# Optimization experiments

Measured on AMD Instinct MI355X. Metric: run time of the kernel, lower is better.

Reference implementation:

```python
import jax, jax.numpy as jnp
import numpy as np

EPS_SUM = 1e-5   # clamp on soft-assignment mass
EPS_NORM = 1e-12  # F.normalize eps


def setup_inputs() -> dict:
    key = jax.random.key(0)
    k1, k2, k3 = jax.random.split(key, 3)
    bs, ch, h, w = 64, 256, 56, 56
    num_parts = 3
    featmaps = jax.random.normal(k1, (bs, ch, h, w), dtype=jnp.float32)
    # kaiming-normal-like init for centers, clamped positive as in init_parameters
    part_centers = jnp.clip(
        jax.random.normal(k2, (num_parts, ch), dtype=jnp.float32) * np.sqrt(2.0 / ch),
        1e-5, None)
    part_smooth_factors = jax.random.normal(k3, (num_parts,), dtype=jnp.float32) * 0.1
    return {"featmaps": featmaps, "part_centers": part_centers,
            "part_smooth_factors": part_smooth_factors}


def reference(featmaps, part_centers, part_smooth_factors):
    bs, ch, h, w = featmaps.shape
    k = part_centers.shape[0]
    x = featmaps.reshape(bs, ch, h * w)                      # [bs, ch, n]

    # distance terms
    cx = jnp.einsum('kc,bcn->bkn', part_centers, x)          # [bs, k, n]
    x_sq = jnp.sum(x * x, axis=1, keepdims=True)             # [bs, 1, n]
    c_sq = jnp.sum(part_centers * part_centers, axis=1)      # [k]

    beta = jax.nn.sigmoid(part_smooth_factors)               # [k]
    logits = jnp.minimum(2.0 * cx - x_sq - c_sq[None, :, None], 0.0) / beta[None, :, None]
    assign = jax.nn.softmax(logits, axis=1)                  # softmax over parts, [bs, k, n]

    # weighted pooling
    qx = jnp.einsum('bkn,bcn->bkc', assign, x)               # [bs, k, ch]
    sum_ass = jnp.maximum(jnp.sum(assign, axis=2, keepdims=True), EPS_SUM)  # [bs, k, 1]
    qx_ = qx / sum_ass

    sigma = jnp.sqrt(beta / 2.0)                             # [k]
    out = (qx_ - part_centers[None]) / sigma[None, :, None]  # [bs, k, ch]
    norm = jnp.maximum(jnp.linalg.norm(out, axis=2, keepdims=True), EPS_NORM)
    outputs = (out / norm).transpose(0, 2, 1)                # [bs, ch, k]

    return outputs, assign.reshape(bs, k, h, w)
```

## Files before the change

kernel.cpp:

```cpp
#include <hip/hip_runtime.h>
#include <math.h>

#define BS   64
#define CH   256
#define NPIX 3136
#define NK   3

#define WS_CSQ   0
#define WS_RB    4
#define WS_CTR4  8
#define WS_SA    (8 + CH*4)
#define WS_QX    (WS_SA + BS*NK)

__global__ __launch_bounds__(64)
void pgn_setup(const float* __restrict__ centers, const float* __restrict__ psf,
               float* __restrict__ ws)
{
    const int lane = threadIdx.x;
    float4* ctr4 = (float4*)(ws + WS_CTR4);
    #pragma unroll
    for (int j = 0; j < 4; ++j) {
        const int c = lane * 4 + j;
        ctr4[c] = make_float4(centers[c], centers[CH + c], centers[2*CH + c], 0.f);
    }
    #pragma unroll
    for (int k = 0; k < NK; ++k) {
        float s = 0.f;
        #pragma unroll
        for (int j = 0; j < 4; ++j) {
            const float u = centers[k*CH + lane*4 + j];
            s = fmaf(u, u, s);
        }
        #pragma unroll
        for (int m = 32; m; m >>= 1) s += __shfl_xor(s, m, 64);
        if (lane == 0) ws[WS_CSQ + k] = s;
    }
    if (lane < NK) ws[WS_RB + lane] = 1.f + __expf(-psf[lane]);
}

#define TILE1 256
#define NT1   13

__global__ __launch_bounds__(256)
void pgn_assign(const float* __restrict__ x,
                const float* __restrict__ ws,
                float* __restrict__ assign_out,
                float* __restrict__ sa)
{
    __shared__ float4 ctr[CH];
    const int tid = threadIdx.x;
    const int b   = blockIdx.x / NT1;
    const int t   = blockIdx.x % NT1;
    const int n   = t * TILE1 + tid;

    ctr[tid] = ((const float4*)(ws + WS_CTR4))[tid];
    __syncthreads();

    const float cs0 = ws[WS_CSQ+0], cs1 = ws[WS_CSQ+1], cs2 = ws[WS_CSQ+2];
    const float rb0 = ws[WS_RB+0],  rb1 = ws[WS_RB+1],  rb2 = ws[WS_RB+2];

    float a0 = 0.f, a1 = 0.f, a2 = 0.f;
    if (n < NPIX) {
        const float* xb = x + (size_t)b * CH * NPIX + n;
        float c0 = 0.f, c1 = 0.f, c2 = 0.f, xs = 0.f;
        #pragma unroll 8
        for (int c = 0; c < CH; ++c) {
            const float  xv = xb[(size_t)c * NPIX];
            const float4 cc = ctr[c];
            c0 = fmaf(cc.x, xv, c0);
            c1 = fmaf(cc.y, xv, c1);
            c2 = fmaf(cc.z, xv, c2);
            xs = fmaf(xv, xv, xs);
        }
        const float l0 = fminf(2.f*c0 - xs - cs0, 0.f) * rb0;
        const float l1 = fminf(2.f*c1 - xs - cs1, 0.f) * rb1;
        const float l2 = fminf(2.f*c2 - xs - cs2, 0.f) * rb2;
        const float m  = fmaxf(l0, fmaxf(l1, l2));
        const float e0 = __expf(l0 - m), e1 = __expf(l1 - m), e2 = __expf(l2 - m);
        const float inv = 1.f / (e0 + e1 + e2);
        a0 = e0 * inv; a1 = e1 * inv; a2 = e2 * inv;

        float* ao = assign_out + (size_t)b * NK * NPIX + n;
        ao[0]        = a0;
        ao[NPIX]     = a1;
        ao[2*NPIX]   = a2;
    }

    float s0 = a0, s1 = a1, s2 = a2;
    #pragma unroll
    for (int m = 32; m; m >>= 1) {
        s0 += __shfl_xor(s0, m, 64);
        s1 += __shfl_xor(s1, m, 64);
        s2 += __shfl_xor(s2, m, 64);
    }
    if ((tid & 63) == 0) {
        atomicAdd(&sa[b*NK + 0], s0);
        atomicAdd(&sa[b*NK + 1], s1);
        atomicAdd(&sa[b*NK + 2], s2);
    }
}

#define CPB 8
#define NCB (CH/CPB)

__global__ __launch_bounds__(256)
void pgn_pool(const float* __restrict__ x,
              const float* __restrict__ assign,
              float* __restrict__ qx)
{
    const int tid = threadIdx.x;
    const int b   = blockIdx.x / NCB;
    const int c0  = (blockIdx.x % NCB) * CPB;

    const float* ab = assign + (size_t)b * NK * NPIX;
    const float* xb = x + ((size_t)b * CH + c0) * NPIX;

    float q[CPB][NK];
    #pragma unroll
    for (int j = 0; j < CPB; ++j)
        #pragma unroll
        for (int k = 0; k < NK; ++k) q[j][k] = 0.f;

    for (int p = tid * 4; p + 3 < NPIX; p += 256 * 4) {
        const float4 A0 = *(const float4*)(ab + p);
        const float4 A1 = *(const float4*)(ab + NPIX + p);
        const float4 A2 = *(const float4*)(ab + 2*NPIX + p);
        #pragma unroll
        for (int j = 0; j < CPB; ++j) {
            const float4 xv = *(const float4*)(xb + (size_t)j * NPIX + p);
            q[j][0] = fmaf(A0.x, xv.x, fmaf(A0.y, xv.y, fmaf(A0.z, xv.z, fmaf(A0.w, xv.w, q[j][0]))));
            q[j][1] = fmaf(A1.x, xv.x, fmaf(A1.y, xv.y, fmaf(A1.z, xv.z, fmaf(A1.w, xv.w, q[j][1]))));
            q[j][2] = fmaf(A2.x, xv.x, fmaf(A2.y, xv.y, fmaf(A2.z, xv.z, fmaf(A2.w, xv.w, q[j][2]))));
        }
    }

    __shared__ float part[4][CPB*NK];
    const int wave = tid >> 6, lane = tid & 63;
    #pragma unroll
    for (int j = 0; j < CPB; ++j)
        #pragma unroll
        for (int k = 0; k < NK; ++k) {
            float v = q[j][k];
            #pragma unroll
            for (int m = 32; m; m >>= 1) v += __shfl_xor(v, m, 64);
            if (lane == 0) part[wave][j*NK + k] = v;
        }
    __syncthreads();
    if (tid < CPB*NK) {
        const float tot = part[0][tid] + part[1][tid] + part[2][tid] + part[3][tid];
        const int j = tid / NK, k = tid % NK;
        qx[((size_t)b*NK + k)*CH + c0 + j] = tot;
    }
}

__global__ __launch_bounds__(256)
void pgn_final(const float* __restrict__ ws,
               const float* __restrict__ centers,
               const float* __restrict__ psf,
               float* __restrict__ out)
{
    const int b = blockIdx.x;
    const int c = threadIdx.x;
    const int wave = c >> 6, lane = c & 63;
    __shared__ float red[4][NK];
    __shared__ float nrm[NK];

    const float* qx = ws + WS_QX;
    const float* sa = ws + WS_SA;

    float v[NK], ss[NK];
    #pragma unroll
    for (int k = 0; k < NK; ++k) {
        const float beta = 1.f / (1.f + __expf(-psf[k]));
        const float sig  = sqrtf(0.5f * beta);
        const float s    = fmaxf(sa[b*NK + k], 1e-5f);
        const float q    = qx[((size_t)b*NK + k)*CH + c] / s;
        v[k]  = (q - centers[k*CH + c]) / sig;
        ss[k] = v[k] * v[k];
    }
    #pragma unroll
    for (int m = 32; m; m >>= 1) {
        ss[0] += __shfl_xor(ss[0], m, 64);
        ss[1] += __shfl_xor(ss[1], m, 64);
        ss[2] += __shfl_xor(ss[2], m, 64);
    }
    if (lane == 0) { red[wave][0] = ss[0]; red[wave][1] = ss[1]; red[wave][2] = ss[2]; }
    __syncthreads();
    if (c < NK) {
        const float tot = red[0][c] + red[1][c] + red[2][c] + red[3][c];
        nrm[c] = fmaxf(sqrtf(tot), 1e-12f);
    }
    __syncthreads();
    float* o = out + ((size_t)b*CH + c)*NK;
    #pragma unroll
    for (int k = 0; k < NK; ++k) o[k] = v[k] / nrm[k];
}

extern "C" void kernel_launch(void* const* d_in, const int* in_sizes, int n_in,
                              void* d_out, int out_size, void* d_ws, size_t ws_size,
                              hipStream_t stream)
{
    const float* feat    = (const float*)d_in[0];
    const float* centers = (const float*)d_in[1];
    const float* psf     = (const float*)d_in[2];

    float* out        = (float*)d_out;
    float* assign_out = out + (size_t)BS*CH*NK;

    float* ws = (float*)d_ws;
    float* sa = ws + WS_SA;
    float* qx = ws + WS_QX;

    hipMemsetAsync(sa, 0, BS*NK*sizeof(float), stream);

    pgn_setup<<<dim3(1), dim3(64), 0, stream>>>(centers, psf, ws);
    pgn_assign<<<dim3(BS*NT1), dim3(256), 0, stream>>>(feat, ws, assign_out, sa);
    pgn_pool<<<dim3(BS*NCB), dim3(256), 0, stream>>>(feat, assign_out, qx);
    pgn_final<<<dim3(BS), dim3(256), 0, stream>>>(ws, centers, psf, out);
}
```

Before: 335.6 us.

## Fuse assignment and pooling into one kernel with shared-memory x tile

Merges the setup, assignment and pooling kernels into a single kernel. Each block loads a 64-pixel by 256-channel tile of featmaps into shared memory once, computes the soft assignment from it, then reuses the same tile for the weighted pooling. Per-block partial qx sums are combined with global atomics. This removes the second full read of featmaps and the re-read of the assign output, at the cost of about 70KB of LDS per block, lower occupancy, and many atomics into qx.

```diff
diff --git a/kernel.cpp b/kernel.cpp
--- a/kernel.cpp
+++ b/kernel.cpp
@@ -5,156 +5,160 @@
 #define CH   256
 #define NPIX 3136
 #define NK   3
-
-#define WS_CSQ   0
-#define WS_RB    4
-#define WS_CTR4  8
-#define WS_SA    (8 + CH*4)
-#define WS_QX    (WS_SA + BS*NK)
-
-__global__ __launch_bounds__(64)
-void pgn_setup(const float* __restrict__ centers, const float* __restrict__ psf,
-               float* __restrict__ ws)
+#define P    64
+#define NT   49
+#define XPAD 68
+
+#define WS_SA 0
+#define WS_QX (BS*NK)
+
+__global__ __launch_bounds__(256)
+void pgn_main(const float* __restrict__ x,
+              const float* __restrict__ centers,
+              const float* __restrict__ psf,
+              float* __restrict__ assign_out,
+              float* __restrict__ sa,
+              float* __restrict__ qx)
 {
-    const int lane = threadIdx.x;
-    float4* ctr4 = (float4*)(ws + WS_CTR4);
+    __shared__ float  x_sh[CH * XPAD];
+    __shared__ float4 ctr_sh[CH];
+    __shared__ float  part[4][16][16];
+    __shared__ float  a_sh[NK][P];
+    __shared__ float  cred[4][NK];
+    __shared__ float  csq_sh[NK];
+
+    const int tid  = threadIdx.x;
+    const int b    = blockIdx.x / NT;
+    const int t    = blockIdx.x % NT;
+    const int n0   = t * P;
+    const int pq   = tid & 15;
+    const int cc   = tid >> 4;
+    const int lane = tid & 63;
+    const int w    = tid >> 6;
+
+    {
+        const float c0 = centers[tid], c1 = centers[CH + tid], c2 = centers[2*CH + tid];
+        ctr_sh[tid] = make_float4(c0, c1, c2, 0.f);
+        float s0 = c0*c0, s1 = c1*c1, s2 = c2*c2;
+        #pragma unroll
+        for (int m = 32; m; m >>= 1) {
+            s0 += __shfl_xor(s0, m, 64);
+            s1 += __shfl_xor(s1, m, 64);
+            s2 += __shfl_xor(s2, m, 64);
+        }
+        if (lane == 0) { cred[w][0] = s0; cred[w][1] = s1; cred[w][2] = s2; }
+    }
+    __syncthreads();
+    if (tid < NK) csq_sh[tid] = cred[0][tid] + cred[1][tid] + cred[2][tid] + cred[3][tid];
+
+    float cxa[NK][4], xsq[4];
+    #pragma unroll
+    for (int j = 0; j < 4; ++j) { cxa[0][j]=0.f; cxa[1][j]=0.f; cxa[2][j]=0.f; xsq[j]=0.f; }
+
+    const float* xb = x + (size_t)b * CH * NPIX + (n0 + 4*pq);
+    #pragma unroll
+    for (int i = 0; i < 16; ++i) {
+        const int c = 16*i + cc;
+        const float4 xv = *(const float4*)(xb + (size_t)c * NPIX);
+        ((float4*)(x_sh + c * XPAD))[pq] = xv;
+        const float4 cv = ctr_sh[c];
+        const float xj[4] = {xv.x, xv.y, xv.z, xv.w};
+        #pragma unroll
+        for (int j = 0; j < 4; ++j) {
+            cxa[0][j] = fmaf(cv.x, xj[j], cxa[0][j]);
+            cxa[1][j] = fmaf(cv.y, xj[j], cxa[1][j]);
+            cxa[2][j] = fmaf(cv.z, xj[j], cxa[2][j]);
+            xsq[j]    = fmaf(xj[j], xj[j], xsq[j]);
+        }
+    }
+
     #pragma unroll
     for (int j = 0; j < 4; ++j) {
-        const int c = lane * 4 + j;
-        ctr4[c] = make_float4(centers[c], centers[CH + c], centers[2*CH + c], 0.f);
-    }
-    #pragma unroll
-    for (int k = 0; k < NK; ++k) {
-        float s = 0.f;
+        #pragma unroll
+        for (int k = 0; k < NK; ++k) {
+            cxa[k][j] += __shfl_xor(cxa[k][j], 16, 64);
+            cxa[k][j] += __shfl_xor(cxa[k][j], 32, 64);
+        }
+        xsq[j] += __shfl_xor(xsq[j], 16, 64);
+        xsq[j] += __shfl_xor(xsq[j], 32, 64);
+    }
+    if ((tid & 48) == 0) {
+        float* pp = &part[w][pq][0];
         #pragma unroll
         for (int j = 0; j < 4; ++j) {
-            const float u = centers[k*CH + lane*4 + j];
-            s = fmaf(u, u, s);
-        }
-        #pragma unroll
-        for (int m = 32; m; m >>= 1) s += __shfl_xor(s, m, 64);
-        if (lane == 0) ws[WS_CSQ + k] = s;
-    }
-    if (lane < NK) ws[WS_RB + lane] = 1.f + __expf(-psf[lane]);
-}
-
-#define TILE1 256
-#define NT1   13
-
-__global__ __launch_bounds__(256)
-void pgn_assign(const float* __restrict__ x,
-                const float* __restrict__ ws,
-                float* __restrict__ assign_out,
-                float* __restrict__ sa)
-{
-    __shared__ float4 ctr[CH];
-    const int tid = threadIdx.x;
-    const int b   = blockIdx.x / NT1;
-    const int t   = blockIdx.x % NT1;
-    const int n   = t * TILE1 + tid;
-
-    ctr[tid] = ((const float4*)(ws + WS_CTR4))[tid];
-    __syncthreads();
-
-    const float cs0 = ws[WS_CSQ+0], cs1 = ws[WS_CSQ+1], cs2 = ws[WS_CSQ+2];
-    const float rb0 = ws[WS_RB+0],  rb1 = ws[WS_RB+1],  rb2 = ws[WS_RB+2];
-
-    float a0 = 0.f, a1 = 0.f, a2 = 0.f;
-    if (n < NPIX) {
-        const float* xb = x + (size_t)b * CH * NPIX + n;
-        float c0 = 0.f, c1 = 0.f, c2 = 0.f, xs = 0.f;
-        #pragma unroll 8
-        for (int c = 0; c < CH; ++c) {
-            const float  xv = xb[(size_t)c * NPIX];
-            const float4 cc = ctr[c];
-            c0 = fmaf(cc.x, xv, c0);
-            c1 = fmaf(cc.y, xv, c1);
-            c2 = fmaf(cc.z, xv, c2);
-            xs = fmaf(xv, xv, xs);
-        }
-        const float l0 = fminf(2.f*c0 - xs - cs0, 0.f) * rb0;
-        const float l1 = fminf(2.f*c1 - xs - cs1, 0.f) * rb1;
-        const float l2 = fminf(2.f*c2 - xs - cs2, 0.f) * rb2;
+            pp[j]      = cxa[0][j];
+            pp[4 + j]  = cxa[1][j];
+            pp[8 + j]  = cxa[2][j];
+            pp[12 + j] = xsq[j];
+        }
+    }
+    __syncthreads();
+
+    if (tid < P) {
+        const int p = tid, q = p >> 2, r = p & 3;
+        float cx0 = 0.f, cx1 = 0.f, cx2 = 0.f, xs = 0.f;
+        #pragma unroll
+        for (int ww = 0; ww < 4; ++ww) {
+            cx0 += part[ww][q][r];
+            cx1 += part[ww][q][4 + r];
+            cx2 += part[ww][q][8 + r];
+            xs  += part[ww][q][12 + r];
+        }
+        const float rb0 = 1.f + __expf(-psf[0]);
+        const float rb1 = 1.f + __expf(-psf[1]);
+        const float rb2 = 1.f + __expf(-psf[2]);
+        const float l0 = fminf(2.f*cx0 - xs - csq_sh[0], 0.f) * rb0;
+        const float l1 = fminf(2.f*cx1 - xs - csq_sh[1], 0.f) * rb1;
+        const float l2 = fminf(2.f*cx2 - xs - csq_sh[2], 0.f) * rb2;
         const float m  = fmaxf(l0, fmaxf(l1, l2));
         const float e0 = __expf(l0 - m), e1 = __expf(l1 - m), e2 = __expf(l2 - m);
         const float inv = 1.f / (e0 + e1 + e2);
-        a0 = e0 * inv; a1 = e1 * inv; a2 = e2 * inv;
-
-        float* ao = assign_out + (size_t)b * NK * NPIX + n;
+        const float a0 = e0*inv, a1 = e1*inv, a2 = e2*inv;
+
+        a_sh[0][p] = a0; a_sh[1][p] = a1; a_sh[2][p] = a2;
+
+        float* ao = assign_out + (size_t)b * NK * NPIX + n0 + p;
         ao[0]        = a0;
         ao[NPIX]     = a1;
         ao[2*NPIX]   = a2;
-    }
-
-    float s0 = a0, s1 = a1, s2 = a2;
-    #pragma unroll
-    for (int m = 32; m; m >>= 1) {
-        s0 += __shfl_xor(s0, m, 64);
-        s1 += __shfl_xor(s1, m, 64);
-        s2 += __shfl_xor(s2, m, 64);
-    }
-    if ((tid & 63) == 0) {
-        atomicAdd(&sa[b*NK + 0], s0);
-        atomicAdd(&sa[b*NK + 1], s1);
-        atomicAdd(&sa[b*NK + 2], s2);
-    }
+
+        float s0 = a0, s1 = a1, s2 = a2;
+        #pragma unroll
+        for (int m2 = 32; m2; m2 >>= 1) {
+            s0 += __shfl_xor(s0, m2, 64);
+            s1 += __shfl_xor(s1, m2, 64);
+            s2 += __shfl_xor(s2, m2, 64);
+        }
+        if (tid == 0) {
+            atomicAdd(&sa[b*NK + 0], s0);
+            atomicAdd(&sa[b*NK + 1], s1);
+            atomicAdd(&sa[b*NK + 2], s2);
+        }
+    }
+    __syncthreads();
+
+    float q0 = 0.f, q1 = 0.f, q2 = 0.f;
+    const float4* xr = (const float4*)(x_sh + tid * XPAD);
+    const float4* A0 = (const float4*)&a_sh[0][0];
+    const float4* A1 = (const float4*)&a_sh[1][0];
+    const float4* A2 = (const float4*)&a_sh[2][0];
+    #pragma unroll
+    for (int i = 0; i < 16; ++i) {
+        const float4 xv  = xr[i];
+        const float4 a0v = A0[i], a1v = A1[i], a2v = A2[i];
+        q0 = fmaf(a0v.x, xv.x, fmaf(a0v.y, xv.y, fmaf(a0v.z, xv.z, fmaf(a0v.w, xv.w, q0))));
+        q1 = fmaf(a1v.x, xv.x, fmaf(a1v.y, xv.y, fmaf(a1v.z, xv.z, fmaf(a1v.w, xv.w, q1))));
+        q2 = fmaf(a2v.x, xv.x, fmaf(a2v.y, xv.y, fmaf(a2v.z, xv.z, fmaf(a2v.w, xv.w, q2))));
+    }
+    float* qb = qx + (size_t)b * NK * CH + tid;
+    atomicAdd(qb,        q0);
+    atomicAdd(qb + CH,   q1);
+    atomicAdd(qb + 2*CH, q2);
 }
 
-#define CPB 8
-#define NCB (CH/CPB)
-
 __global__ __launch_bounds__(256)
-void pgn_pool(const float* __restrict__ x,
-              const float* __restrict__ assign,
-              float* __restrict__ qx)
-{
-    const int tid = threadIdx.x;
-    const int b   = blockIdx.x / NCB;
-    const int c0  = (blockIdx.x % NCB) * CPB;
-
-    const float* ab = assign + (size_t)b * NK * NPIX;
-    const float* xb = x + ((size_t)b * CH + c0) * NPIX;
-
-    float q[CPB][NK];
-    #pragma unroll
-    for (int j = 0; j < CPB; ++j)
-        #pragma unroll
-        for (int k = 0; k < NK; ++k) q[j][k] = 0.f;
-
-    for (int p = tid * 4; p + 3 < NPIX; p += 256 * 4) {
-        const float4 A0 = *(const float4*)(ab + p);
-        const float4 A1 = *(const float4*)(ab + NPIX + p);
-        const float4 A2 = *(const float4*)(ab + 2*NPIX + p);
-        #pragma unroll
-        for (int j = 0; j < CPB; ++j) {
-            const float4 xv = *(const float4*)(xb + (size_t)j * NPIX + p);
-            q[j][0] = fmaf(A0.x, xv.x, fmaf(A0.y, xv.y, fmaf(A0.z, xv.z, fmaf(A0.w, xv.w, q[j][0]))));
-            q[j][1] = fmaf(A1.x, xv.x, fmaf(A1.y, xv.y, fmaf(A1.z, xv.z, fmaf(A1.w, xv.w, q[j][1]))));
-            q[j][2] = fmaf(A2.x, xv.x, fmaf(A2.y, xv.y, fmaf(A2.z, xv.z, fmaf(A2.w, xv.w, q[j][2]))));
-        }
-    }
-
-    __shared__ float part[4][CPB*NK];
-    const int wave = tid >> 6, lane = tid & 63;
-    #pragma unroll
-    for (int j = 0; j < CPB; ++j)
-        #pragma unroll
-        for (int k = 0; k < NK; ++k) {
-            float v = q[j][k];
-            #pragma unroll
-            for (int m = 32; m; m >>= 1) v += __shfl_xor(v, m, 64);
-            if (lane == 0) part[wave][j*NK + k] = v;
-        }
-    __syncthreads();
-    if (tid < CPB*NK) {
-        const float tot = part[0][tid] + part[1][tid] + part[2][tid] + part[3][tid];
-        const int j = tid / NK, k = tid % NK;
-        qx[((size_t)b*NK + k)*CH + c0 + j] = tot;
-    }
-}
-
-__global__ __launch_bounds__(256)
-void pgn_final(const float* __restrict__ ws,
+void pgn_final(const float* __restrict__ qx,
+               const float* __restrict__ sa,
                const float* __restrict__ centers,
                const float* __restrict__ psf,
                float* __restrict__ out)
@@ -165,9 +169,6 @@
     __shared__ float red[4][NK];
     __shared__ float nrm[NK];
 
-    const float* qx = ws + WS_QX;
-    const float* sa = ws + WS_SA;
-
     float v[NK], ss[NK];
     #pragma unroll
     for (int k = 0; k < NK; ++k) {
@@ -207,14 +208,13 @@
     float* out        = (float*)d_out;
     float* assign_out = out + (size_t)BS*CH*NK;
 
-    float* ws = (float*)d_ws;
-    float* sa = ws + WS_SA;
-    float* qx = ws + WS_QX;
-
-    hipMemsetAsync(sa, 0, BS*NK*sizeof(float), stream);
-
-    pgn_setup<<<dim3(1), dim3(64), 0, stream>>>(centers, psf, ws);
-    pgn_assign<<<dim3(BS*NT1), dim3(256), 0, stream>>>(feat, ws, assign_out, sa);
-    pgn_pool<<<dim3(BS*NCB), dim3(256), 0, stream>>>(feat, assign_out, qx);
-    pgn_final<<<dim3(BS), dim3(256), 0, stream>>>(ws, centers, psf, out);
+    float* sa = (float*)d_ws + WS_SA;
+    float* qx = (float*)d_ws + WS_QX;
+
+    hipMemsetAsync(d_ws, 0, (BS*NK + BS*NK*CH) * sizeof(float), stream);
+
+    pgn_main<<<dim3(BS*NT), dim3(256), 0, stream>>>(
+        feat, centers, psf, assign_out, sa, qx);
+
+    pgn_final<<<dim3(BS), dim3(256), 0, stream>>>(qx, sa, centers, psf, out);
 }
```

After: 299.3 us. -10.8%, faster.
